# Kernel tuning notes

Hardware: AMD Instinct MI355X
Metric: run time of the kernel (lower is better)

Reference implementation:

```python
import jax, jax.numpy as jnp
import numpy as np

UFEAT_DIM = 256
MAPFEAT_DIM = 64


def setup_inputs() -> dict:
    key = jax.random.key(0)
    k1, k2, k3, k4 = jax.random.split(key, 4)
    ufeat = jax.random.normal(k1, (32, 512, UFEAT_DIM), dtype=jnp.float32)
    mapfeat = jax.random.normal(k2, (32, 4096, MAPFEAT_DIM), dtype=jnp.float32)
    # weight_norm(Linear, dim=None): W = g * V / ||V||_F, g scalar
    v_w = jax.random.normal(k3, (MAPFEAT_DIM, UFEAT_DIM), dtype=jnp.float32) * 0.05
    g = jnp.asarray(1.0, dtype=jnp.float32)
    b = jax.random.normal(k4, (MAPFEAT_DIM,), dtype=jnp.float32) * 0.05
    return {"ufeat": ufeat, "mapfeat": mapfeat, "v_w": v_w, "g": g, "b": b}


def reference(ufeat, mapfeat, v_w, g, b):
    # weight-normalized linear (dim=None -> scalar g over Frobenius norm)
    w = g * v_w / jnp.linalg.norm(v_w)
    proj = jax.nn.relu(jnp.einsum("bud,md->bum", ufeat, w) + b)  # [B, U, M]
    norm = jnp.sqrt(jnp.asarray(MAPFEAT_DIM, dtype=proj.dtype))
    # broadcast dot-product over spatial map, expressed as a batched matmul
    logit = jnp.einsum("bum,bsm->bus", proj, mapfeat) / norm  # [B, U, x*y]
    return logit
```

## Files before the change

### kernel.cpp

```cpp
#include <hip/hip_runtime.h>
#include <hip/hip_bf16.h>

typedef __bf16 bf16x8 __attribute__((ext_vector_type(8)));
typedef float  f32x16 __attribute__((ext_vector_type(16)));
typedef float  f32x4  __attribute__((ext_vector_type(4)));

#define UF_D 256
#define MAP_M 64
#define B_DIM 32
#define U_DIM 512
#define S_DIM 4096

__global__ __launch_bounds__(256) void prep_conv_kernel(
    const float* __restrict__ v_w, const float* __restrict__ g,
    const float* __restrict__ b, const float* __restrict__ mapfeat,
    __bf16* __restrict__ w_bf16, float* __restrict__ b_s,
    __bf16* __restrict__ map_bf16)
{
    const int t = threadIdx.x;
    if (blockIdx.x == 0) {
        __shared__ float red[256];
        const f32x4* v4 = (const f32x4*)v_w;
        float ss = 0.f;
        for (int i = t; i < 4096; i += 256) {
            f32x4 v = v4[i];
            ss += v.x * v.x + v.y * v.y + v.z * v.z + v.w * v.w;
        }
        red[t] = ss;
        __syncthreads();
        for (int s = 128; s > 0; s >>= 1) {
            if (t < s) red[t] += red[t + s];
            __syncthreads();
        }
        const float scale = g[0] / (sqrtf(red[0]) * 8.0f);
        for (int i = t; i < 4096; i += 256) {
            f32x4 v = v4[i];
            w_bf16[4 * i + 0] = (__bf16)(v.x * scale);
            w_bf16[4 * i + 1] = (__bf16)(v.y * scale);
            w_bf16[4 * i + 2] = (__bf16)(v.z * scale);
            w_bf16[4 * i + 3] = (__bf16)(v.w * scale);
        }
        if (t < MAP_M) b_s[t] = b[t] * 0.125f;
    } else {
        const int NC = (B_DIM * S_DIM * MAP_M) / 8;
        const f32x4* m4 = (const f32x4*)mapfeat;
        bf16x8* o8 = (bf16x8*)map_bf16;
        for (int c = (blockIdx.x - 1) * 256 + t; c < NC; c += 255 * 256) {
            f32x4 q0 = __builtin_nontemporal_load(&m4[2 * c]);
            f32x4 q1 = __builtin_nontemporal_load(&m4[2 * c + 1]);
            bf16x8 o;
            o[0] = (__bf16)q0.x; o[1] = (__bf16)q0.y;
            o[2] = (__bf16)q0.z; o[3] = (__bf16)q0.w;
            o[4] = (__bf16)q1.x; o[5] = (__bf16)q1.y;
            o[6] = (__bf16)q1.z; o[7] = (__bf16)q1.w;
            o8[c] = o;
        }
    }
}

__global__ __launch_bounds__(256) void proj_kernel(
    const float* __restrict__ ufeat,
    const __bf16* __restrict__ w,
    const float* __restrict__ b_s,
    __bf16* __restrict__ proj)
{
    const int wave = threadIdx.x >> 6;
    const int lane = threadIdx.x & 63;
    const int r  = lane & 31;
    const int kh = lane >> 5;
    const int wr = wave >> 1, wc = wave & 1;
    const int row0 = blockIdx.x * 64 + wr * 32;
    const int col0 = wc * 32;

    f32x16 acc = {};
    const float*  ap = ufeat + (size_t)(row0 + r) * UF_D + kh * 8;
    const __bf16* wp = w + (col0 + r) * UF_D + kh * 8;

#pragma unroll
    for (int k = 0; k < UF_D; k += 16) {
        f32x4 a01 = *(const f32x4*)(ap + k);
        f32x4 a23 = *(const f32x4*)(ap + k + 4);
        bf16x8 af;
        af[0] = (__bf16)a01.x; af[1] = (__bf16)a01.y;
        af[2] = (__bf16)a01.z; af[3] = (__bf16)a01.w;
        af[4] = (__bf16)a23.x; af[5] = (__bf16)a23.y;
        af[6] = (__bf16)a23.z; af[7] = (__bf16)a23.w;
        bf16x8 wf = *(const bf16x8*)(wp + k);
        acc = __builtin_amdgcn_mfma_f32_32x32x16_bf16(af, wf, acc, 0, 0, 0);
    }

#pragma unroll
    for (int j = 0; j < 16; ++j) {
        const int rl = (j & 3) + 8 * (j >> 2) + 4 * kh;
        const size_t row = row0 + rl;
        const int col = col0 + r;
        float v = acc[j] + b_s[col];
        proj[row * MAP_M + col] = (__bf16)fmaxf(v, 0.f);
    }
}

__global__ __launch_bounds__(256) void logit_kernel(
    const __bf16* __restrict__ proj,
    const __bf16* __restrict__ map,
    float* __restrict__ out)
{
    const int vid = (blockIdx.x & 7) * 512 + (blockIdx.x >> 3);
    const int ut = vid & 15;
    const int st = (vid >> 4) & 7;
    const int b  = vid >> 7;

    const int wave = threadIdx.x >> 6;
    const int lane = threadIdx.x & 63;
    const int r  = lane & 31;
    const int kh = lane >> 5;

    const int u0 = ut * 32;
    const int s0 = st * 512 + wave * 128;

    const __bf16* A  = proj + (size_t)b * U_DIM * MAP_M;
    const __bf16* Bm = map  + (size_t)b * S_DIM * MAP_M;

    f32x16 acc0 = {}, acc1 = {}, acc2 = {}, acc3 = {};

    const __bf16* ap  = A  + (size_t)(u0 + r) * MAP_M + kh * 8;
    const __bf16* bp0 = Bm + (size_t)(s0 +   0 + r) * MAP_M + kh * 8;
    const __bf16* bp1 = Bm + (size_t)(s0 +  32 + r) * MAP_M + kh * 8;
    const __bf16* bp2 = Bm + (size_t)(s0 +  64 + r) * MAP_M + kh * 8;
    const __bf16* bp3 = Bm + (size_t)(s0 +  96 + r) * MAP_M + kh * 8;

#pragma unroll
    for (int k = 0; k < MAP_M; k += 16) {
        bf16x8 a  = *(const bf16x8*)(ap  + k);
        bf16x8 f0 = *(const bf16x8*)(bp0 + k);
        bf16x8 f1 = *(const bf16x8*)(bp1 + k);
        bf16x8 f2 = *(const bf16x8*)(bp2 + k);
        bf16x8 f3 = *(const bf16x8*)(bp3 + k);
        acc0 = __builtin_amdgcn_mfma_f32_32x32x16_bf16(a, f0, acc0, 0, 0, 0);
        acc1 = __builtin_amdgcn_mfma_f32_32x32x16_bf16(a, f1, acc1, 0, 0, 0);
        acc2 = __builtin_amdgcn_mfma_f32_32x32x16_bf16(a, f2, acc2, 0, 0, 0);
        acc3 = __builtin_amdgcn_mfma_f32_32x32x16_bf16(a, f3, acc3, 0, 0, 0);
    }

    float* O = out + (size_t)b * U_DIM * S_DIM;
#pragma unroll
    for (int j = 0; j < 16; ++j) {
        const int rl = (j & 3) + 8 * (j >> 2) + 4 * kh;
        const size_t row = u0 + rl;
        float* orow = O + row * S_DIM + s0 + r;
        __builtin_nontemporal_store(acc0[j], orow);
        __builtin_nontemporal_store(acc1[j], orow + 32);
        __builtin_nontemporal_store(acc2[j], orow + 64);
        __builtin_nontemporal_store(acc3[j], orow + 96);
    }
}

extern "C" void kernel_launch(void* const* d_in, const int* in_sizes, int n_in,
                              void* d_out, int out_size, void* d_ws, size_t ws_size,
                              hipStream_t stream) {
    const float* ufeat   = (const float*)d_in[0];
    const float* mapfeat = (const float*)d_in[1];
    const float* v_w     = (const float*)d_in[2];
    const float* g       = (const float*)d_in[3];
    const float* b       = (const float*)d_in[4];
    float* out = (float*)d_out;

    __bf16* w_bf16   = (__bf16*)d_ws;
    float*  b_s      = (float*)((char*)d_ws + 32768);
    __bf16* proj     = (__bf16*)((char*)d_ws + 65536);
    __bf16* map_bf16 = (__bf16*)((char*)d_ws + 65536 + 2097152);

    prep_conv_kernel<<<256, 256, 0, stream>>>(v_w, g, b, mapfeat, w_bf16, b_s, map_bf16);
    proj_kernel<<<256, 256, 0, stream>>>(ufeat, w_bf16, b_s, proj);
    logit_kernel<<<B_DIM * 8 * 16, 256, 0, stream>>>(proj, map_bf16, out);
}
```

Baseline: 326.5 us.

## Fuse weight-norm prep with projection GEMM and double u-tiles per logit block

Merges the prep kernel and the projection kernel into one launch. Each of the 256 projection blocks recomputes the Frobenius norm of v_w and applies the weight-norm scale and bias in its epilogue, reading fp32 weights directly. Another 256 blocks convert mapfeat to bf16 in parallel. This removes one launch and the w_bf16/b_s round-trip, at the cost of redundant norm reductions. The logit kernel now covers two 32-row u-tiles per block with half the blocks, reusing the map tile loads across both.

```diff
diff --git a/kernel.cpp b/kernel.cpp
--- a/kernel.cpp
+++ b/kernel.cpp
@@ -11,15 +11,37 @@
 #define U_DIM 512
 #define S_DIM 4096
 
-__global__ __launch_bounds__(256) void prep_conv_kernel(
-    const float* __restrict__ v_w, const float* __restrict__ g,
-    const float* __restrict__ b, const float* __restrict__ mapfeat,
-    __bf16* __restrict__ w_bf16, float* __restrict__ b_s,
+__global__ __launch_bounds__(256) void fused_prep_proj_kernel(
+    const float* __restrict__ ufeat,
+    const float* __restrict__ v_w,
+    const float* __restrict__ g,
+    const float* __restrict__ b,
+    const float* __restrict__ mapfeat,
+    __bf16* __restrict__ proj,
     __bf16* __restrict__ map_bf16)
 {
     const int t = threadIdx.x;
-    if (blockIdx.x == 0) {
-        __shared__ float red[256];
+
+    if (blockIdx.x >= 256) {
+        const int cid = blockIdx.x - 256;
+        const int NC = (B_DIM * S_DIM * MAP_M) / 8;
+        const f32x4* m4 = (const f32x4*)mapfeat;
+        bf16x8* o8 = (bf16x8*)map_bf16;
+        for (int c = cid * 256 + t; c < NC; c += 256 * 256) {
+            f32x4 q0 = __builtin_nontemporal_load(&m4[2 * c]);
+            f32x4 q1 = __builtin_nontemporal_load(&m4[2 * c + 1]);
+            bf16x8 o;
+            o[0] = (__bf16)q0.x; o[1] = (__bf16)q0.y;
+            o[2] = (__bf16)q0.z; o[3] = (__bf16)q0.w;
+            o[4] = (__bf16)q1.x; o[5] = (__bf16)q1.y;
+            o[6] = (__bf16)q1.z; o[7] = (__bf16)q1.w;
+            o8[c] = o;
+        }
+        return;
+    }
+
+    __shared__ float red[256];
+    {
         const f32x4* v4 = (const f32x4*)v_w;
         float ss = 0.f;
         for (int i = t; i < 4096; i += 256) {
@@ -32,40 +54,11 @@
             if (t < s) red[t] += red[t + s];
             __syncthreads();
         }
-        const float scale = g[0] / (sqrtf(red[0]) * 8.0f);
-        for (int i = t; i < 4096; i += 256) {
-            f32x4 v = v4[i];
-            w_bf16[4 * i + 0] = (__bf16)(v.x * scale);
-            w_bf16[4 * i + 1] = (__bf16)(v.y * scale);
-            w_bf16[4 * i + 2] = (__bf16)(v.z * scale);
-            w_bf16[4 * i + 3] = (__bf16)(v.w * scale);
-        }
-        if (t < MAP_M) b_s[t] = b[t] * 0.125f;
-    } else {
-        const int NC = (B_DIM * S_DIM * MAP_M) / 8;
-        const f32x4* m4 = (const f32x4*)mapfeat;
-        bf16x8* o8 = (bf16x8*)map_bf16;
-        for (int c = (blockIdx.x - 1) * 256 + t; c < NC; c += 255 * 256) {
-            f32x4 q0 = __builtin_nontemporal_load(&m4[2 * c]);
-            f32x4 q1 = __builtin_nontemporal_load(&m4[2 * c + 1]);
-            bf16x8 o;
-            o[0] = (__bf16)q0.x; o[1] = (__bf16)q0.y;
-            o[2] = (__bf16)q0.z; o[3] = (__bf16)q0.w;
-            o[4] = (__bf16)q1.x; o[5] = (__bf16)q1.y;
-            o[6] = (__bf16)q1.z; o[7] = (__bf16)q1.w;
-            o8[c] = o;
-        }
     }
-}
+    const float s8 = g[0] / (sqrtf(red[0]) * 8.0f);
 
-__global__ __launch_bounds__(256) void proj_kernel(
-    const float* __restrict__ ufeat,
-    const __bf16* __restrict__ w,
-    const float* __restrict__ b_s,
-    __bf16* __restrict__ proj)
-{
-    const int wave = threadIdx.x >> 6;
-    const int lane = threadIdx.x & 63;
+    const int wave = t >> 6;
+    const int lane = t & 63;
     const int r  = lane & 31;
     const int kh = lane >> 5;
     const int wr = wave >> 1, wc = wave & 1;
@@ -73,19 +66,24 @@
     const int col0 = wc * 32;
 
     f32x16 acc = {};
-    const float*  ap = ufeat + (size_t)(row0 + r) * UF_D + kh * 8;
-    const __bf16* wp = w + (col0 + r) * UF_D + kh * 8;
+    const float* ap = ufeat + (size_t)(row0 + r) * UF_D + kh * 8;
+    const float* wp = v_w   + (size_t)(col0 + r) * UF_D + kh * 8;
 
 #pragma unroll
     for (int k = 0; k < UF_D; k += 16) {
         f32x4 a01 = *(const f32x4*)(ap + k);
         f32x4 a23 = *(const f32x4*)(ap + k + 4);
-        bf16x8 af;
+        f32x4 w01 = *(const f32x4*)(wp + k);
+        f32x4 w23 = *(const f32x4*)(wp + k + 4);
+        bf16x8 af, wf;
         af[0] = (__bf16)a01.x; af[1] = (__bf16)a01.y;
         af[2] = (__bf16)a01.z; af[3] = (__bf16)a01.w;
         af[4] = (__bf16)a23.x; af[5] = (__bf16)a23.y;
         af[6] = (__bf16)a23.z; af[7] = (__bf16)a23.w;
-        bf16x8 wf = *(const bf16x8*)(wp + k);
+        wf[0] = (__bf16)w01.x; wf[1] = (__bf16)w01.y;
+        wf[2] = (__bf16)w01.z; wf[3] = (__bf16)w01.w;
+        wf[4] = (__bf16)w23.x; wf[5] = (__bf16)w23.y;
+        wf[6] = (__bf16)w23.z; wf[7] = (__bf16)w23.w;
         acc = __builtin_amdgcn_mfma_f32_32x32x16_bf16(af, wf, acc, 0, 0, 0);
     }
 
@@ -94,7 +92,7 @@
         const int rl = (j & 3) + 8 * (j >> 2) + 4 * kh;
         const size_t row = row0 + rl;
         const int col = col0 + r;
-        float v = acc[j] + b_s[col];
+        float v = acc[j] * s8 + b[col] * 0.125f;
         proj[row * MAP_M + col] = (__bf16)fmaxf(v, 0.f);
     }
 }
@@ -104,53 +102,57 @@
     const __bf16* __restrict__ map,
     float* __restrict__ out)
 {
-    const int vid = (blockIdx.x & 7) * 512 + (blockIdx.x >> 3);
-    const int ut = vid & 15;
-    const int st = (vid >> 4) & 7;
-    const int b  = vid >> 7;
+    const int vid = (blockIdx.x & 7) * 256 + (blockIdx.x >> 3);
+    const int utp = vid & 7;
+    const int st  = (vid >> 3) & 7;
+    const int b   = vid >> 6;
 
     const int wave = threadIdx.x >> 6;
     const int lane = threadIdx.x & 63;
     const int r  = lane & 31;
     const int kh = lane >> 5;
 
-    const int u0 = ut * 32;
     const int s0 = st * 512 + wave * 128;
 
     const __bf16* A  = proj + (size_t)b * U_DIM * MAP_M;
     const __bf16* Bm = map  + (size_t)b * S_DIM * MAP_M;
+    float* O = out + (size_t)b * U_DIM * S_DIM;
 
-    f32x16 acc0 = {}, acc1 = {}, acc2 = {}, acc3 = {};
-
-    const __bf16* ap  = A  + (size_t)(u0 + r) * MAP_M + kh * 8;
     const __bf16* bp0 = Bm + (size_t)(s0 +   0 + r) * MAP_M + kh * 8;
     const __bf16* bp1 = Bm + (size_t)(s0 +  32 + r) * MAP_M + kh * 8;
     const __bf16* bp2 = Bm + (size_t)(s0 +  64 + r) * MAP_M + kh * 8;
     const __bf16* bp3 = Bm + (size_t)(s0 +  96 + r) * MAP_M + kh * 8;
 
 #pragma unroll
-    for (int k = 0; k < MAP_M; k += 16) {
-        bf16x8 a  = *(const bf16x8*)(ap  + k);
-        bf16x8 f0 = *(const bf16x8*)(bp0 + k);
-        bf16x8 f1 = *(const bf16x8*)(bp1 + k);
-        bf16x8 f2 = *(const bf16x8*)(bp2 + k);
-        bf16x8 f3 = *(const bf16x8*)(bp3 + k);
-        acc0 = __builtin_amdgcn_mfma_f32_32x32x16_bf16(a, f0, acc0, 0, 0, 0);
-        acc1 = __builtin_amdgcn_mfma_f32_32x32x16_bf16(a, f1, acc1, 0, 0, 0);
-        acc2 = __builtin_amdgcn_mfma_f32_32x32x16_bf16(a, f2, acc2, 0, 0, 0);
-        acc3 = __builtin_amdgcn_mfma_f32_32x32x16_bf16(a, f3, acc3, 0, 0, 0);
-    }
+    for (int t2 = 0; t2 < 2; ++t2) {
+        const int u0 = (utp * 2 + t2) * 32;
+        const __bf16* ap = A + (size_t)(u0 + r) * MAP_M + kh * 8;
 
-    float* O = out + (size_t)b * U_DIM * S_DIM;
+        f32x16 acc0 = {}, acc1 = {}, acc2 = {}, acc3 = {};
+
 #pragma unroll
-    for (int j = 0; j < 16; ++j) {
-        const int rl = (j & 3) + 8 * (j >> 2) + 4 * kh;
-        const size_t row = u0 + rl;
-        float* orow = O + row * S_DIM + s0 + r;
-        __builtin_nontemporal_store(acc0[j], orow);
-        __builtin_nontemporal_store(acc1[j], orow + 32);
-        __builtin_nontemporal_store(acc2[j], orow + 64);
-        __builtin_nontemporal_store(acc3[j], orow + 96);
+        for (int k = 0; k < MAP_M; k += 16) {
+            bf16x8 a  = *(const bf16x8*)(ap  + k);
+            bf16x8 f0 = *(const bf16x8*)(bp0 + k);
+            bf16x8 f1 = *(const bf16x8*)(bp1 + k);
+            bf16x8 f2 = *(const bf16x8*)(bp2 + k);
+            bf16x8 f3 = *(const bf16x8*)(bp3 + k);
+            acc0 = __builtin_amdgcn_mfma_f32_32x32x16_bf16(a, f0, acc0, 0, 0, 0);
+            acc1 = __builtin_amdgcn_mfma_f32_32x32x16_bf16(a, f1, acc1, 0, 0, 0);
+            acc2 = __builtin_amdgcn_mfma_f32_32x32x16_bf16(a, f2, acc2, 0, 0, 0);
+            acc3 = __builtin_amdgcn_mfma_f32_32x32x16_bf16(a, f3, acc3, 0, 0, 0);
+        }
+
+#pragma unroll
+        for (int j = 0; j < 16; ++j) {
+            const int rl = (j & 3) + 8 * (j >> 2) + 4 * kh;
+            const size_t row = u0 + rl;
+            float* orow = O + row * S_DIM + s0 + r;
+            __builtin_nontemporal_store(acc0[j], orow);
+            __builtin_nontemporal_store(acc1[j], orow + 32);
+            __builtin_nontemporal_store(acc2[j], orow + 64);
+            __builtin_nontemporal_store(acc3[j], orow + 96);
+        }
     }
 }
 
@@ -164,12 +166,10 @@
     const float* b       = (const float*)d_in[4];
     float* out = (float*)d_out;
 
-    __bf16* w_bf16   = (__bf16*)d_ws;
-    float*  b_s      = (float*)((char*)d_ws + 32768);
-    __bf16* proj     = (__bf16*)((char*)d_ws + 65536);
-    __bf16* map_bf16 = (__bf16*)((char*)d_ws + 65536 + 2097152);
+    __bf16* proj     = (__bf16*)d_ws;
+    __bf16* map_bf16 = (__bf16*)((char*)d_ws + 2097152);
 
-    prep_conv_kernel<<<256, 256, 0, stream>>>(v_w, g, b, mapfeat, w_bf16, b_s, map_bf16);
-    proj_kernel<<<256, 256, 0, stream>>>(ufeat, w_bf16, b_s, proj);
-    logit_kernel<<<B_DIM * 8 * 16, 256, 0, stream>>>(proj, map_bf16, out);
+    fused_prep_proj_kernel<<<512, 256, 0, stream>>>(ufeat, v_w, g, b, mapfeat,
+                                                    proj, map_bf16);
+    logit_kernel<<<2048, 256, 0, stream>>>(proj, map_bf16, out);
 }
```

Result: no change. 327.1 us (+0.2%).
